# Performance work log

Measured on AMD Instinct MI355X. Metric: run time of the kernel, lower is better.

Reference implementation:

```python
import jax, jax.numpy as jnp
import numpy as np

N, E = 50000, 400000
IN_DIM = OUT_DIM = 256
H, DK = 8, 32
NT, ET = 6, 3
LN_EPS = 1e-5


def setup_inputs() -> dict:
    key = jax.random.key(0)
    ks = jax.random.split(key, 16)
    glorot = lambda k, shape: jax.random.normal(k, shape, jnp.float32) * np.sqrt(2.0 / (shape[-2] + shape[-1]))
    return {
        "node_features": jax.random.normal(ks[0], (N, IN_DIM), jnp.float32),
        "edge_index": jax.random.randint(ks[1], (2, E), 0, N, jnp.int32),
        "edge_features": jax.random.normal(ks[2], (E, 16), jnp.float32),
        "node_types": jax.random.randint(ks[3], (N,), 0, NT, jnp.int32),
        "edge_types": jax.random.randint(ks[4], (E,), 0, ET, jnp.int32),
        # type-specific projection weights stored [T, in, out] (y = x @ W + b)
        "Wk": glorot(ks[5], (NT, IN_DIM, OUT_DIM)), "bk": jnp.zeros((NT, OUT_DIM), jnp.float32),
        "Wq": glorot(ks[6], (NT, IN_DIM, OUT_DIM)), "bq": jnp.zeros((NT, OUT_DIM), jnp.float32),
        "Wv": glorot(ks[7], (NT, IN_DIM, OUT_DIM)), "bv": jnp.zeros((NT, OUT_DIM), jnp.float32),
        "relation_pri": jnp.ones((ET, H), jnp.float32),
        # relation transforms, no bias, stored [T, dk_in, dk_out]
        "Wa": glorot(ks[8], (ET, DK, DK)),
        "Wm": glorot(ks[9], (ET, DK, DK)),
        "ln_g": jnp.ones((OUT_DIM,), jnp.float32),
        "ln_b": jnp.zeros((OUT_DIM,), jnp.float32),
    }


def _type_proj(x, node_types, W, b):
    # compute all 6 type projections, then select per node (faithful to masked loop)
    y_all = jnp.einsum("ni,tio->tno", x, W) + b[:, None, :]  # [T, N, out]
    return y_all[node_types, jnp.arange(x.shape[0])]         # [N, out]


def _forward(node_features, edge_index, node_types, edge_types,
             Wk, bk, Wq, bq, Wv, bv, relation_pri, Wa, Wm, ln_g, ln_b):
    n = node_features.shape[0]
    K = _type_proj(node_features, node_types, Wk, bk).reshape(n, H, DK)
    Q = _type_proj(node_features, node_types, Wq, bq).reshape(n, H, DK)
    V = _type_proj(node_features, node_types, Wv, bv).reshape(n, H, DK)

    src, tgt = edge_index[0], edge_index[1]
    Ks, Qt, Vs = K[src], Q[tgt], V[src]  # [E, H, dk]
    inv_sqrt_dk = 1.0 / np.sqrt(DK).astype(np.float32)

    msgs = jnp.zeros((edge_types.shape[0], H, DK), jnp.float32)
    for t in range(ET):  # small fixed loop over edge types
        mask = edge_types == t                              # [E]
        Ke = jnp.einsum("ehd,dk->ehk", Ks, Wa[t])           # relation_att
        Ve = jnp.einsum("ehd,dk->ehk", Vs, Wm[t])           # relation_msg
        scores = jnp.sum(Ke * Qt, -1) * inv_sqrt_dk * relation_pri[t]  # [E, H]
        scores = jnp.where(mask[:, None], scores, -jnp.inf)
        w = jax.nn.softmax(scores, axis=0)                  # softmax over ALL edges of this type
        msgs = msgs + jnp.where(mask[:, None, None], w[..., None] * Ve, 0.0)

    agg = jax.ops.segment_sum(msgs.reshape(-1, OUT_DIM), tgt, num_segments=n)  # index_add_
    out = agg + node_features                               # skip = Identity (in_dim == out_dim)
    mu = jnp.mean(out, -1, keepdims=True)
    var = jnp.var(out, -1, keepdims=True)
    return (out - mu) * jax.lax.rsqrt(var + LN_EPS) * ln_g + ln_b


def reference(node_features, edge_index, edge_features, node_types, edge_types,
              Wk, bk, Wq, bq, Wv, bv, relation_pri, Wa, Wm, ln_g, ln_b):
    # edge_features are unused by the original forward; dropout is eval-mode identity
    return _forward(node_features, edge_index, node_types, edge_types,
                    Wk, bk, Wq, bq, Wv, bv, relation_pri, Wa, Wm, ln_g, ln_b)
```

## Files before the change

kernel.cpp:

```cpp
#include <hip/hip_runtime.h>
#include <math.h>

#define H_    8
#define DK_   32
#define NT_   6
#define ET_   3
#define DIM_  256
#define LN_EPS 1e-5f
#define NMATS (NT_ * 7)
#define NBLK  2048
#define NBIN  (ET_ * H_)
#define NSTEP 56
#define TROWS 128
#define MAXNB 1024

typedef __attribute__((ext_vector_type(8))) short short8v;
typedef __attribute__((ext_vector_type(4))) float f32x4;
typedef __attribute__((ext_vector_type(2))) float f32x2;

__device__ __forceinline__ unsigned short f2bf(float f){
    unsigned u = __float_as_uint(f);
    return (unsigned short)((u + 0x7fffu + ((u >> 16) & 1u)) >> 16);
}
__device__ __forceinline__ float bflo(unsigned u){ return __uint_as_float(u << 16); }
__device__ __forceinline__ float bfhi(unsigned u){ return __uint_as_float(u & 0xFFFF0000u); }

__device__ __forceinline__ unsigned char f2fp8(float f){
    int r = __builtin_amdgcn_cvt_pk_fp8_f32(f, f, 0, false);
    return (unsigned char)(r & 0xFF);
}

__global__ __launch_bounds__(256) void k_hist(const int* __restrict__ ntyp, int n,
                                              int* __restrict__ bhist){
    const int tid = threadIdx.x;
    const int gi = blockIdx.x * 256 + tid;
    const int wave = tid >> 6, lane = tid & 63;
    const int t = (gi < n) ? ntyp[gi] : -1;
    __shared__ int whist[4][8];
    #pragma unroll
    for (int tt = 0; tt < NT_; tt++){
        unsigned long long bal = __ballot(t == tt);
        if (lane == 0) whist[wave][tt] = __popcll(bal);
    }
    __syncthreads();
    if (tid < NT_)
        bhist[blockIdx.x * 8 + tid] =
            whist[0][tid] + whist[1][tid] + whist[2][tid] + whist[3][tid];
}

__global__ __launch_bounds__(256) void k_scanhist(int* __restrict__ bhist, int nb,
                                                  int* __restrict__ offs, int* __restrict__ meta){
    __shared__ int hh[MAXNB * 8 / 4];
    __shared__ int tot[8], toff[8], tbase[8], ntl_s;
    const int tid = threadIdx.x;

    for (int i = tid; i < nb * 8; i += 256) hh[i] = bhist[i];
    __syncthreads();

    if (tid < 8){
        int run = 0;
        for (int b = 0; b < nb; b++){
            int c = hh[b * 8 + tid];
            hh[b * 8 + tid] = run;
            run += c;
        }
        tot[tid] = run;
    }
    __syncthreads();

    if (tid == 0){
        int off = 0, tb = 0;
        for (int tt = 0; tt < NT_; tt++){
            toff[tt] = off;
            tbase[tt] = tb;
            tb += (tot[tt] + TROWS - 1) / TROWS;
            off += tot[tt];
        }
        for (int tt = NT_; tt < 8; tt++){ toff[tt] = 0; tbase[tt] = tb; }
        ntl_s = tb;
        meta[0] = tb;
    }
    __syncthreads();

    for (int i = tid; i < ntl_s; i += 256){
        int t = 0;
        #pragma unroll
        for (int tt = 1; tt < NT_; tt++) if (i >= tbase[tt]) t = tt;
        const int k = i - tbase[t];
        const int rem = tot[t] - k * TROWS;
        meta[1 + 3*i]     = t;
        meta[1 + 3*i + 1] = toff[t] + k * TROWS;
        meta[1 + 3*i + 2] = (rem < TROWS) ? rem : TROWS;
    }
    if (tid < NT_) offs[tid] = toff[tid];

    for (int i = tid; i < nb * 8; i += 256)
        bhist[i] = hh[i] + toff[i & 7];
}

__global__ __launch_bounds__(256) void k_scatter2(const int* __restrict__ ntyp, int n,
                                                  const int* __restrict__ bhist,
                                                  int* __restrict__ sorted){
    const int tid = threadIdx.x;
    const int gi = blockIdx.x * 256 + tid;
    const int wave = tid >> 6, lane = tid & 63;
    const int t = (gi < n) ? ntyp[gi] : -1;
    __shared__ int whist[4][8];
    unsigned long long mybal = 0;
    #pragma unroll
    for (int tt = 0; tt < NT_; tt++){
        unsigned long long bal = __ballot(t == tt);
        if (lane == 0) whist[wave][tt] = __popcll(bal);
        if (t == tt) mybal = bal;
    }
    __syncthreads();
    if (gi < n){
        int wo = 0;
        for (int w = 0; w < wave; w++) wo += whist[w][t];
        const unsigned long long below = (lane == 0) ? 0ULL : (~0ULL >> (64 - lane));
        const int rank = bhist[blockIdx.x * 8 + t] + wo + __popcll(mybal & below);
        sorted[rank] = gi;
    }
}

__global__ __launch_bounds__(256) void k_pack(
    const float* __restrict__ Wq, const float* __restrict__ Wk, const float* __restrict__ Wv,
    const float* __restrict__ Wa, const float* __restrict__ Wm, const float* __restrict__ pri,
    unsigned short* __restrict__ pw)
{
    const int gid = blockIdx.x * 256 + threadIdx.x;
    if (gid >= NMATS * 8 * 16 * 64) return;
    const int l = gid & 63;
    const int j = (gid >> 6) & 15;
    const int p = (gid >> 10) & 7;
    const int matg = gid >> 13;
    const int tn = matg / 7, m = matg % 7;
    const int col = j * 16 + (l & 15);
    const int k0  = p * 32 + (l >> 4) * 8;
    const int h = col >> 5, c = col & 31;

    float vals[8];
    if (m == 0){
        #pragma unroll
        for (int i = 0; i < 8; i++)
            vals[i] = Wq[((size_t)tn * 256 + (k0 + i)) * 256 + col];
    } else if (m <= 3){
        const int te = m - 1;
        const float scale = 0.17677669529663687f * pri[te * H_ + h];
        #pragma unroll
        for (int i = 0; i < 8; i++){
            const float* wk = Wk + ((size_t)tn * 256 + (k0 + i)) * 256 + h * 32;
            const float* wa = Wa + (size_t)te * 1024 + c;
            float s = 0.f;
            for (int d = 0; d < 32; d++) s = fmaf(wk[d], wa[d * 32], s);
            vals[i] = s * scale;
        }
    } else {
        const int te = m - 4;
        #pragma unroll
        for (int i = 0; i < 8; i++){
            const float* wv = Wv + ((size_t)tn * 256 + (k0 + i)) * 256 + h * 32;
            const float* wm = Wm + (size_t)te * 1024 + c;
            float s = 0.f;
            for (int d = 0; d < 32; d++) s = fmaf(wv[d], wm[d * 32], s);
            vals[i] = s;
        }
    }
    unsigned short o[8];
    #pragma unroll
    for (int i = 0; i < 8; i++) o[i] = f2bf(vals[i]);
    *reinterpret_cast<uint4*>(pw + (size_t)gid * 8) = *reinterpret_cast<const uint4*>(o);
}

__global__ void k_bias(
    const float* __restrict__ bq, const float* __restrict__ bk, const float* __restrict__ bv,
    const float* __restrict__ Wa, const float* __restrict__ Wm, const float* __restrict__ pri,
    float* __restrict__ bpack)
{
    const int gid = blockIdx.x * 256 + threadIdx.x;
    if (gid >= NMATS * 256) return;
    const int col = gid & 255;
    const int matg = gid >> 8;
    const int tn = matg / 7, m = matg % 7;
    const int h = col >> 5, c = col & 31;
    float v;
    if (m == 0) v = bq[tn * 256 + col];
    else if (m <= 3){
        const int te = m - 1;
        float s = 0.f;
        for (int d = 0; d < 32; d++) s = fmaf(bk[tn * 256 + h * 32 + d], Wa[te * 1024 + d * 32 + c], s);
        v = s * 0.17677669529663687f * pri[te * H_ + h];
    } else {
        const int te = m - 4;
        float s = 0.f;
        for (int d = 0; d < 32; d++) s = fmaf(bv[tn * 256 + h * 32 + d], Wm[te * 1024 + d * 32 + c], s);
        v = s;
    }
    bpack[gid] = v;
}

__global__ __launch_bounds__(512, 2) void k_proj(
    const float* __restrict__ x, const int* __restrict__ sorted, const int* __restrict__ meta,
    const unsigned short* __restrict__ pw, const float* __restrict__ bpack,
    unsigned short* __restrict__ Qb, unsigned char* __restrict__ Ktb, unsigned char* __restrict__ Vtb)
{
    const int ntl = meta[0];
    if ((int)blockIdx.x >= ntl) return;
    const int q = ntl >> 3, r = ntl & 7;
    const int xcd = blockIdx.x & 7, ii = blockIdx.x >> 3;
    const int tile = (xcd < r) ? xcd * (q + 1) + ii
                               : r * (q + 1) + (xcd - r) * q + ii;
    const int tn    = meta[1 + 3*tile];
    const int start = meta[1 + 3*tile + 1];
    const int rows  = meta[1 + 3*tile + 2];

    __shared__ unsigned short xs[TROWS * 256];
    __shared__ int ids[TROWS];
    const int tid = threadIdx.x;
    if (tid < TROWS) ids[tid] = sorted[start + ((tid < rows) ? tid : 0)];
    __syncthreads();

    char* xb = reinterpret_cast<char*>(xs);
    for (int idx = tid; idx < TROWS * 32; idx += 512){
        const int r2 = idx >> 5, c16 = idx & 31;
        const float* src = x + (size_t)ids[r2] * DIM_ + c16 * 8;
        float4 a = *reinterpret_cast<const float4*>(src);
        float4 b = *reinterpret_cast<const float4*>(src + 4);
        unsigned short o[8] = {f2bf(a.x), f2bf(a.y), f2bf(a.z), f2bf(a.w),
                               f2bf(b.x), f2bf(b.y), f2bf(b.z), f2bf(b.w)};
        const int byte = r2 * 512 + ((c16 * 16) ^ ((r2 & 7) << 4));
        *reinterpret_cast<uint4*>(xb + byte) = *reinterpret_cast<const uint4*>(o);
    }
    __syncthreads();

    const int wid = tid >> 6, l = tid & 63;
    const int rg = wid >> 2;
    const int cg = wid & 3;
    const int l15 = l & 15, lg = l >> 4;
    const int xorv = (l15 & 7) << 4;
    const size_t matbase = (size_t)tn * 7;
    const int rowbase = rg * 64;

    f32x4 acc[4][4];
    short8v b0[4], b1[4];

    {
        const unsigned short* sp0 = pw + matbase * 8 * 8192;
        #pragma unroll
        for (int j = 0; j < 4; j++)
            b0[j] = *reinterpret_cast<const short8v*>(sp0 + (cg * 4 + j) * 512 + l * 8);
    }

    auto proj_step = [&](const int s, short8v (&cur)[4], short8v (&pf)[4]){
        const int m = s >> 3, p = s & 7;
        const int matg = (int)matbase + m;

        if (s + 1 < NSTEP){
            const unsigned short* sp = pw + (matbase * 8 + (s + 1)) * 8192;
            #pragma unroll
            for (int j = 0; j < 4; j++)
                pf[j] = *reinterpret_cast<const short8v*>(sp + (cg * 4 + j) * 512 + l * 8);
        }

        if (p == 0){
            #pragma unroll
            for (int j = 0; j < 4; j++){
                const float bj = bpack[matg * 256 + cg * 64 + j * 16 + l15];
                #pragma unroll
                for (int i = 0; i < 4; i++) acc[i][j] = (f32x4){bj, bj, bj, bj};
            }
        }

        {
            short8v a[4];
            const int kb = (p * 64 + (lg << 4)) ^ xorv;
            #pragma unroll
            for (int i = 0; i < 4; i++)
                a[i] = *reinterpret_cast<const short8v*>(xb + (rowbase + i * 16 + l15) * 512 + kb);
            #pragma unroll
            for (int i = 0; i < 4; i++)
                #pragma unroll
                for (int j = 0; j < 4; j++)
                    acc[i][j] = __builtin_amdgcn_mfma_f32_16x16x32_bf16(a[i], cur[j], acc[i][j], 0, 0, 0);
        }

        if (p == 7){
            #pragma unroll
            for (int i = 0; i < 4; i++){
                #pragma unroll
                for (int rr = 0; rr < 4; rr++){
                    const int row = rowbase + i * 16 + lg * 4 + rr;
                    if (row < rows){
                        const size_t node = (size_t)ids[row];
                        if (m == 0){
                            unsigned short* optr = Qb + node * 256 + cg * 64 + l15;
                            #pragma unroll
                            for (int j = 0; j < 4; j++) optr[j * 16] = f2bf(acc[i][j][rr]);
                        } else {
                            unsigned char* optr = ((m <= 3) ? Ktb + node * 768 + (size_t)(m - 1) * 256
                                                            : Vtb + node * 768 + (size_t)(m - 4) * 256)
                                                  + cg * 64 + l15;
                            #pragma unroll
                            for (int j = 0; j < 4; j++) optr[j * 16] = f2fp8(acc[i][j][rr]);
                        }
                    }
                }
            }
        }
    };

    for (int s = 0; s < NSTEP; s += 2){
        proj_step(s,     b0, b1);
        proj_step(s + 1, b1, b0);
    }
}

__global__ void k_ecount(const int* __restrict__ ei, int E_, int* __restrict__ ecnt){
    int e = blockIdx.x * blockDim.x + threadIdx.x;
    if (e < E_) atomicAdd(&ecnt[ei[E_ + e]], 1);
}

__global__ __launch_bounds__(256) void k_scan1(const int* __restrict__ ecnt, int n,
                                               int* __restrict__ excl, int* __restrict__ bsum){
    __shared__ int sh[256];
    const int tid = threadIdx.x;
    const int gi = blockIdx.x * 256 + tid;
    int v = (gi < n) ? ecnt[gi] : 0;
    sh[tid] = v;
    __syncthreads();
    for (int off = 1; off < 256; off <<= 1){
        int t = (tid >= off) ? sh[tid - off] : 0;
        __syncthreads();
        sh[tid] += t;
        __syncthreads();
    }
    if (gi < n) excl[gi] = sh[tid] - v;
    if (tid == 255) bsum[blockIdx.x] = sh[255];
}

__global__ __launch_bounds__(256) void k_scan2(int* __restrict__ bsum, int nb){
    __shared__ int sh[MAXNB];
    const int tid = threadIdx.x;
    for (int i = tid; i < nb; i += 256) sh[i] = bsum[i];
    __syncthreads();
    if (tid == 0){
        int run = 0;
        for (int b = 0; b < nb; b++){ int c = sh[b]; sh[b] = run; run += c; }
    }
    __syncthreads();
    for (int i = tid; i < nb; i += 256) bsum[i] = sh[i];
}

__global__ __launch_bounds__(256) void k_scan3(int n, int E_, const int* __restrict__ bsum,
                                               int* __restrict__ eoff, int* __restrict__ cursor){
    const int gi = blockIdx.x * 256 + threadIdx.x;
    if (gi < n){
        int v = eoff[gi] + bsum[blockIdx.x];
        eoff[gi] = v;
        cursor[gi] = v;
    }
    if (gi == 0) eoff[n] = E_;
}

__global__ void k_escatter(const int* __restrict__ ei, const int* __restrict__ etyp, int E_,
                           int* __restrict__ cursor, int2* __restrict__ ep){
    int e = blockIdx.x * blockDim.x + threadIdx.x;
    if (e < E_){
        int tg = ei[E_ + e];
        int pos = atomicAdd(&cursor[tg], 1);
        ep[pos] = make_int2(ei[e] | (etyp[e] << 28), tg);
    }
}

__global__ __launch_bounds__(256) void k_score(
    const unsigned char* __restrict__ Ktb, const unsigned short* __restrict__ Qb,
    const int2* __restrict__ ep,
    float* __restrict__ SC, float* __restrict__ psum, int EH)
{
    const int tid = threadIdx.x;
    float s0 = 0.f, s1 = 0.f, s2 = 0.f;

    for (int idx = blockIdx.x * 256 + tid; idx < EH; idx += NBLK * 256){
        const int pos = idx >> 3, h = idx & 7;
        const int2 pr = ep[pos];
        const int s = pr.x & 0x0FFFFFFF, t = pr.x >> 28;
        const int tg = pr.y;
        const unsigned char*  kp = Ktb + ((size_t)s * 3 + t) * 256 + h * 32;
        const unsigned short* qp = Qb + (size_t)tg * 256 + h * 32;
        uint4 k8a = *reinterpret_cast<const uint4*>(kp);
        uint4 k8b = *reinterpret_cast<const uint4*>(kp + 16);
        unsigned kw[8] = {k8a.x, k8a.y, k8a.z, k8a.w, k8b.x, k8b.y, k8b.z, k8b.w};
        uint4 qa = *reinterpret_cast<const uint4*>(qp);
        uint4 qb = *reinterpret_cast<const uint4*>(qp + 8);
        uint4 qc = *reinterpret_cast<const uint4*>(qp + 16);
        uint4 qd = *reinterpret_cast<const uint4*>(qp + 24);
        unsigned qw[16] = {qa.x, qa.y, qa.z, qa.w, qb.x, qb.y, qb.z, qb.w,
                           qc.x, qc.y, qc.z, qc.w, qd.x, qd.y, qd.z, qd.w};
        float acc = 0.f;
        #pragma unroll
        for (int w = 0; w < 8; w++){
            f32x2 lo = __builtin_amdgcn_cvt_pk_f32_fp8(kw[w], false);
            f32x2 hi = __builtin_amdgcn_cvt_pk_f32_fp8(kw[w], true);
            acc = fmaf(lo.x, bflo(qw[2*w]),   acc);
            acc = fmaf(lo.y, bfhi(qw[2*w]),   acc);
            acc = fmaf(hi.x, bflo(qw[2*w+1]), acc);
            acc = fmaf(hi.y, bfhi(qw[2*w+1]), acc);
        }
        const float e = __expf(acc);
        SC[idx] = e;
        s0 += (t == 0) ? e : 0.f;
        s1 += (t == 1) ? e : 0.f;
        s2 += (t == 2) ? e : 0.f;
    }

    #pragma unroll
    for (int s = 8; s <= 32; s <<= 1){
        s0 += __shfl_xor(s0, s, 64);
        s1 += __shfl_xor(s1, s, 64);
        s2 += __shfl_xor(s2, s, 64);
    }
    __shared__ float sm[4][NBIN];
    const int wave = tid >> 6, lane = tid & 63;
    if (lane < 8){ sm[wave][lane] = s0; sm[wave][8 + lane] = s1; sm[wave][16 + lane] = s2; }
    __syncthreads();
    if (tid < NBIN)
        psum[blockIdx.x * NBIN + tid] = sm[0][tid] + sm[1][tid] + sm[2][tid] + sm[3][tid];
}

__global__ __launch_bounds__(256) void k_redsum(const float* __restrict__ psum,
                                                float* __restrict__ rw){
    const int b = blockIdx.x, tid = threadIdx.x;
    float s = 0.f;
    for (int i = tid; i < NBLK; i += 256) s += psum[i * NBIN + b];
    #pragma unroll
    for (int m = 1; m < 64; m <<= 1) s += __shfl_xor(s, m, 64);
    __shared__ float sm[4];
    if ((tid & 63) == 0) sm[tid >> 6] = s;
    __syncthreads();
    if (tid == 0){
        float t = sm[0] + sm[1] + sm[2] + sm[3];
        rw[b] = (t > 0.f) ? 1.f / t : 0.f;
    }
}

__global__ __launch_bounds__(256) void k_aggln(
    const unsigned char* __restrict__ Vtb, const float* __restrict__ x,
    const int* __restrict__ eoff, const int2* __restrict__ ep,
    const float* __restrict__ SC, const float* __restrict__ rw,
    const float* __restrict__ g, const float* __restrict__ b,
    float* __restrict__ out, int n)
{
    const int idx = blockIdx.x * 256 + threadIdx.x;
    if (idx >= n * H_) return;
    const int tg = idx >> 3, h = idx & 7;

    const float rw0 = rw[h], rw1 = rw[8 + h], rw2 = rw[16 + h];

    float acc[DK_];
    #pragma unroll
    for (int k = 0; k < DK_; k++) acc[k] = 0.f;

    const int p1 = eoff[tg + 1];
    for (int pos = eoff[tg]; pos < p1; ++pos){
        const int pl = ep[pos].x;
        const int s = pl & 0x0FFFFFFF, t = pl >> 28;
        const float rwv = (t == 0) ? rw0 : (t == 1) ? rw1 : rw2;
        const float w = SC[pos * 8 + h] * rwv;
        const unsigned char* vp = Vtb + ((size_t)s * 3 + t) * 256 + h * 32;
        uint4 v8a = *reinterpret_cast<const uint4*>(vp);
        uint4 v8b = *reinterpret_cast<const uint4*>(vp + 16);
        unsigned vw[8] = {v8a.x, v8a.y, v8a.z, v8a.w, v8b.x, v8b.y, v8b.z, v8b.w};
        #pragma unroll
        for (int q = 0; q < 8; q++){
            f32x2 lo = __builtin_amdgcn_cvt_pk_f32_fp8(vw[q], false);
            f32x2 hi = __builtin_amdgcn_cvt_pk_f32_fp8(vw[q], true);
            acc[4*q+0] = fmaf(w, lo.x, acc[4*q+0]);
            acc[4*q+1] = fmaf(w, lo.y, acc[4*q+1]);
            acc[4*q+2] = fmaf(w, hi.x, acc[4*q+2]);
            acc[4*q+3] = fmaf(w, hi.y, acc[4*q+3]);
        }
    }

    #pragma unroll
    for (int k4 = 0; k4 < 8; k4++){
        float4 x4 = *reinterpret_cast<const float4*>(x + (size_t)tg * DIM_ + h * DK_ + k4 * 4);
        acc[4*k4] += x4.x; acc[4*k4+1] += x4.y; acc[4*k4+2] += x4.z; acc[4*k4+3] += x4.w;
    }

    float s1 = 0.f, s2 = 0.f;
    #pragma unroll
    for (int k = 0; k < DK_; k++){ s1 += acc[k]; s2 = fmaf(acc[k], acc[k], s2); }
    #pragma unroll
    for (int m = 1; m <= 4; m <<= 1){
        s1 += __shfl_xor(s1, m, 64);
        s2 += __shfl_xor(s2, m, 64);
    }
    const float mu  = s1 * (1.f / DIM_);
    const float var = s2 * (1.f / DIM_) - mu * mu;
    const float rs  = rsqrtf(var + LN_EPS);

    float* __restrict__ o = out + (size_t)tg * DIM_ + h * DK_;
    #pragma unroll
    for (int k4 = 0; k4 < 8; k4++){
        float4 g4 = *reinterpret_cast<const float4*>(g + h * DK_ + k4 * 4);
        float4 b4 = *reinterpret_cast<const float4*>(b + h * DK_ + k4 * 4);
        float4 o4;
        o4.x = (acc[4*k4]   - mu) * rs * g4.x + b4.x;
        o4.y = (acc[4*k4+1] - mu) * rs * g4.y + b4.y;
        o4.z = (acc[4*k4+2] - mu) * rs * g4.z + b4.z;
        o4.w = (acc[4*k4+3] - mu) * rs * g4.w + b4.w;
        *reinterpret_cast<float4*>(o + k4 * 4) = o4;
    }
}

extern "C" void kernel_launch(void* const* d_in, const int* in_sizes, int n_in,
                              void* d_out, int out_size, void* d_ws, size_t ws_size,
                              hipStream_t stream)
{
    const float* x   = (const float*)d_in[0];
    const int*  ei   = (const int*)d_in[1];
    const int*  ntyp = (const int*)d_in[3];
    const int*  etyp = (const int*)d_in[4];
    const float* Wk  = (const float*)d_in[5];
    const float* bk  = (const float*)d_in[6];
    const float* Wq  = (const float*)d_in[7];
    const float* bq  = (const float*)d_in[8];
    const float* Wv  = (const float*)d_in[9];
    const float* bv  = (const float*)d_in[10];
    const float* pri = (const float*)d_in[11];
    const float* Wa  = (const float*)d_in[12];
    const float* Wm  = (const float*)d_in[13];
    const float* lg  = (const float*)d_in[14];
    const float* lb  = (const float*)d_in[15];

    const int n  = in_sizes[0] / DIM_;
    const int E_ = in_sizes[4];
    const int EH = E_ * H_;
    float* out = (float*)d_out;

    const size_t NF = (size_t)n * DIM_;
    unsigned short* Qb  = (unsigned short*)d_ws;
    unsigned char*  Ktb = (unsigned char*)(Qb + NF);
    unsigned char*  Vtb = Ktb + NF * 3;
    unsigned short* pwp = (unsigned short*)(Vtb + NF * 3);
    float* SC    = (float*)(pwp + (size_t)NMATS * 65536);
    float* bpack = SC + (size_t)EH;
    float* psum  = bpack + NMATS * 256;
    float* rw    = psum + (size_t)NBLK * NBIN;
    int* sorted  = (int*)(rw + NBIN);
    int* offsN   = sorted + n;
    const int NB = (n + 255) / 256;
    int* bhist   = offsN + 8;
    int* meta    = bhist + (size_t)NB * 8;
    const int maxtiles = (n + TROWS - 1) / TROWS + NT_;
    int* ecnt    = meta + 1 + 3 * maxtiles;
    int* eoff    = ecnt + n;
    int* cursorE = eoff + n + 1;
    int* bsum    = cursorE + n;
    int2* ep     = (int2*)(bsum + 1024);

    hipMemsetAsync(ecnt, 0, (size_t)n * sizeof(int), stream);

    k_pack<<<(NMATS * 8 * 16 * 64 + 255) / 256, 256, 0, stream>>>(Wq, Wk, Wv, Wa, Wm, pri, pwp);
    k_bias<<<(NMATS * 256 + 255) / 256, 256, 0, stream>>>(bq, bk, bv, Wa, Wm, pri, bpack);

    k_hist    <<<NB, 256, 0, stream>>>(ntyp, n, bhist);
    k_scanhist<<<1, 256, 0, stream>>>(bhist, NB, offsN, meta);
    k_scatter2<<<NB, 256, 0, stream>>>(ntyp, n, bhist, sorted);
    k_proj    <<<maxtiles, 512, 0, stream>>>(x, sorted, meta, pwp, bpack, Qb, Ktb, Vtb);

    k_ecount  <<<(E_ + 255) / 256, 256, 0, stream>>>(ei, E_, ecnt);
    k_scan1   <<<NB, 256, 0, stream>>>(ecnt, n, eoff, bsum);
    k_scan2   <<<1, 256, 0, stream>>>(bsum, NB);
    k_scan3   <<<NB, 256, 0, stream>>>(n, E_, bsum, eoff, cursorE);
    k_escatter<<<(E_ + 255) / 256, 256, 0, stream>>>(ei, etyp, E_, cursorE, ep);

    k_score <<<NBLK, 256, 0, stream>>>(Ktb, Qb, ep, SC, psum, EH);
    k_redsum<<<NBIN, 256, 0, stream>>>(psum, rw);
    k_aggln <<<(n * H_ + 255) / 256, 256, 0, stream>>>(Vtb, x, eoff, ep, SC, rw, lg, lb, out, n);
}
```

Before: 244.0 us.

## Assign one wavefront per target node in aggregation and store scores as bf16

The aggregation kernel now gives each target node a full 64-lane wave: 8 edge slots by 8 heads, with lanes striding over incoming edges. Partial 32-wide accumulators are then combined across edge slots with cross-lane shuffles, and only lane group 0 writes the normalized output. This raises parallelism and hides gather latency for nodes with many edges, at the cost of 8x more threads, many shuffles and idle lanes on low-degree nodes. Separately, the exp scores are stored in bf16 instead of fp32, halving that buffer's traffic at some precision cost.

```diff
diff --git a/kernel.cpp b/kernel.cpp
--- a/kernel.cpp
+++ b/kernel.cpp
@@ -24,6 +24,7 @@
 }
 __device__ __forceinline__ float bflo(unsigned u){ return __uint_as_float(u << 16); }
 __device__ __forceinline__ float bfhi(unsigned u){ return __uint_as_float(u & 0xFFFF0000u); }
+__device__ __forceinline__ float bf2f(unsigned short v){ return __uint_as_float((unsigned)v << 16); }
 
 __device__ __forceinline__ unsigned char f2fp8(float f){
     int r = __builtin_amdgcn_cvt_pk_fp8_f32(f, f, 0, false);
@@ -375,7 +376,7 @@
 __global__ __launch_bounds__(256) void k_score(
     const unsigned char* __restrict__ Ktb, const unsigned short* __restrict__ Qb,
     const int2* __restrict__ ep,
-    float* __restrict__ SC, float* __restrict__ psum, int EH)
+    unsigned short* __restrict__ SC, float* __restrict__ psum, int EH)
 {
     const int tid = threadIdx.x;
     float s0 = 0.f, s1 = 0.f, s2 = 0.f;
@@ -407,7 +408,7 @@
             acc = fmaf(hi.y, bfhi(qw[2*w+1]), acc);
         }
         const float e = __expf(acc);
-        SC[idx] = e;
+        SC[idx] = f2bf(e);
         s0 += (t == 0) ? e : 0.f;
         s1 += (t == 1) ? e : 0.f;
         s2 += (t == 2) ? e : 0.f;
@@ -446,13 +447,15 @@
 __global__ __launch_bounds__(256) void k_aggln(
     const unsigned char* __restrict__ Vtb, const float* __restrict__ x,
     const int* __restrict__ eoff, const int2* __restrict__ ep,
-    const float* __restrict__ SC, const float* __restrict__ rw,
+    const unsigned short* __restrict__ SC, const float* __restrict__ rw,
     const float* __restrict__ g, const float* __restrict__ b,
     float* __restrict__ out, int n)
 {
-    const int idx = blockIdx.x * 256 + threadIdx.x;
-    if (idx >= n * H_) return;
-    const int tg = idx >> 3, h = idx & 7;
+    const int gw = (blockIdx.x * 256 + threadIdx.x) >> 6;
+    if (gw >= n) return;
+    const int lane = threadIdx.x & 63;
+    const int el = lane >> 3, h = lane & 7;
+    const int tg = gw;
 
     const float rw0 = rw[h], rw1 = rw[8 + h], rw2 = rw[16 + h];
 
@@ -460,12 +463,12 @@
     #pragma unroll
     for (int k = 0; k < DK_; k++) acc[k] = 0.f;
 
-    const int p1 = eoff[tg + 1];
-    for (int pos = eoff[tg]; pos < p1; ++pos){
+    const int p0 = eoff[tg], p1 = eoff[tg + 1];
+    for (int pos = p0 + el; pos < p1; pos += 8){
         const int pl = ep[pos].x;
         const int s = pl & 0x0FFFFFFF, t = pl >> 28;
         const float rwv = (t == 0) ? rw0 : (t == 1) ? rw1 : rw2;
-        const float w = SC[pos * 8 + h] * rwv;
+        const float w = bf2f(SC[pos * 8 + h]) * rwv;
         const unsigned char* vp = Vtb + ((size_t)s * 3 + t) * 256 + h * 32;
         uint4 v8a = *reinterpret_cast<const uint4*>(vp);
         uint4 v8b = *reinterpret_cast<const uint4*>(vp + 16);
@@ -482,6 +485,11 @@
     }
 
     #pragma unroll
+    for (int m = 8; m <= 32; m <<= 1)
+        #pragma unroll
+        for (int k = 0; k < DK_; k++) acc[k] += __shfl_xor(acc[k], m, 64);
+
+    #pragma unroll
     for (int k4 = 0; k4 < 8; k4++){
         float4 x4 = *reinterpret_cast<const float4*>(x + (size_t)tg * DIM_ + h * DK_ + k4 * 4);
         acc[4*k4] += x4.x; acc[4*k4+1] += x4.y; acc[4*k4+2] += x4.z; acc[4*k4+3] += x4.w;
@@ -499,17 +507,19 @@
     const float var = s2 * (1.f / DIM_) - mu * mu;
     const float rs  = rsqrtf(var + LN_EPS);
 
-    float* __restrict__ o = out + (size_t)tg * DIM_ + h * DK_;
-    #pragma unroll
-    for (int k4 = 0; k4 < 8; k4++){
-        float4 g4 = *reinterpret_cast<const float4*>(g + h * DK_ + k4 * 4);
-        float4 b4 = *reinterpret_cast<const float4*>(b + h * DK_ + k4 * 4);
-        float4 o4;
-        o4.x = (acc[4*k4]   - mu) * rs * g4.x + b4.x;
-        o4.y = (acc[4*k4+1] - mu) * rs * g4.y + b4.y;
-        o4.z = (acc[4*k4+2] - mu) * rs * g4.z + b4.z;
-        o4.w = (acc[4*k4+3] - mu) * rs * g4.w + b4.w;
-        *reinterpret_cast<float4*>(o + k4 * 4) = o4;
+    if (el == 0){
+        float* __restrict__ o = out + (size_t)tg * DIM_ + h * DK_;
+        #pragma unroll
+        for (int k4 = 0; k4 < 8; k4++){
+            float4 g4 = *reinterpret_cast<const float4*>(g + h * DK_ + k4 * 4);
+            float4 b4 = *reinterpret_cast<const float4*>(b + h * DK_ + k4 * 4);
+            float4 o4;
+            o4.x = (acc[4*k4]   - mu) * rs * g4.x + b4.x;
+            o4.y = (acc[4*k4+1] - mu) * rs * g4.y + b4.y;
+            o4.z = (acc[4*k4+2] - mu) * rs * g4.z + b4.z;
+            o4.w = (acc[4*k4+3] - mu) * rs * g4.w + b4.w;
+            *reinterpret_cast<float4*>(o + k4 * 4) = o4;
+        }
     }
 }
 
@@ -543,8 +553,8 @@
     unsigned char*  Ktb = (unsigned char*)(Qb + NF);
     unsigned char*  Vtb = Ktb + NF * 3;
     unsigned short* pwp = (unsigned short*)(Vtb + NF * 3);
-    float* SC    = (float*)(pwp + (size_t)NMATS * 65536);
-    float* bpack = SC + (size_t)EH;
+    unsigned short* SC  = pwp + (size_t)NMATS * 65536;
+    float* bpack = (float*)(SC + (size_t)EH);
     float* psum  = bpack + NMATS * 256;
     float* rw    = psum + (size_t)NBLK * NBIN;
     int* sorted  = (int*)(rw + NBIN);
@@ -577,5 +587,5 @@
 
     k_score <<<NBLK, 256, 0, stream>>>(Ktb, Qb, ep, SC, psum, EH);
     k_redsum<<<NBIN, 256, 0, stream>>>(psum, rw);
-    k_aggln <<<(n * H_ + 255) / 256, 256, 0, stream>>>(Vtb, x, eoff, ep, SC, rw, lg, lb, out, n);
-}
+    k_aggln <<<(n * 64 + 255) / 256, 256, 0, stream>>>(Vtb, x, eoff, ep, SC, rw, lg, lb, out, n);
+}
```

Result: slower. 284.8 us (+16.7%).
